# Optimization experiments

Hardware: AMD Instinct MI355X
Metric: run time of the kernel (lower is better)

Reference implementation:

```python
import jax, jax.numpy as jnp
import numpy as np

B, S, E, H = 2, 2048, 1024, 16
D = E // H  # head_dim = 64
EPS = 1e-6


def _angle_decay():
    # angle: 1/10000**linspace(0,1,D//2), each value repeated twice (interleaved)
    a = 1.0 / (10000.0 ** jnp.linspace(0.0, 1.0, D // 2))
    angle = jnp.repeat(a, 2)  # [D]
    decay = jnp.log(1.0 - 2.0 ** (-5.0 - jnp.arange(H, dtype=jnp.float32)))  # [H]
    return angle, decay


def _rel_pos(slen):
    angle, decay = _angle_decay()
    idx = jnp.arange(slen, dtype=jnp.float32)
    sin = jnp.sin(idx[:, None] * angle[None, :])  # [S, D]
    cos = jnp.cos(idx[:, None] * angle[None, :])  # [S, D]
    diff = idx[:, None] - idx[None, :]            # [S, S]
    tril = diff >= 0
    masked = jnp.where(tril, diff, jnp.inf)
    mask = jnp.exp(masked * decay[:, None, None])  # [H, S, S]; exp(-inf)=0 on upper tri
    mask = jnp.nan_to_num(mask)
    mask = mask / jnp.sqrt(jnp.sum(mask, axis=-1, keepdims=True))
    return sin, cos, mask


def _rotate_every_two(x):
    x1 = x[..., ::2]
    x2 = x[..., 1::2]
    return jnp.stack((-x2, x1), axis=-1).reshape(x.shape)


def _theta_shift(x, sin, cos):
    # x: [B, H, S, D]; sin/cos: [S, D] broadcast over B,H
    return x * cos + _rotate_every_two(x) * sin


def setup_inputs() -> dict:
    key = jax.random.key(0)
    ks = jax.random.split(key, 5)
    scale = 1.0 / np.sqrt(E)
    return {
        "x": jax.random.normal(ks[0], (B, S, E), dtype=jnp.float32),
        "Wq": jax.random.normal(ks[1], (E, E), dtype=jnp.float32) * scale,
        "Wk": jax.random.normal(ks[2], (E, E), dtype=jnp.float32) * scale,
        "Wv": jax.random.normal(ks[3], (E, E), dtype=jnp.float32) * scale,
        "Wg": jax.random.normal(ks[4], (E, E), dtype=jnp.float32) * scale,
    }


def reference(x, Wq, Wk, Wv, Wg):
    bsz, tgt_len, _ = x.shape
    sin, cos, mask = _rel_pos(tgt_len)
    scaling = E ** (-0.5)

    q = x @ Wq
    k = (x @ Wk) * scaling
    v = x @ Wv
    g = x @ Wg

    q = q.reshape(bsz, tgt_len, H, D).transpose(0, 2, 1, 3)  # [B,H,S,D]
    k = k.reshape(bsz, tgt_len, H, D).transpose(0, 2, 1, 3)
    vr = v.reshape(bsz, tgt_len, H, D).transpose(0, 2, 1, 3)

    qr = _theta_shift(q, sin, cos)
    kr = _theta_shift(k, sin, cos)

    qk = jnp.einsum("bhqd,bhkd->bhqk", qr, kr) * mask[None]
    denom = jax.lax.stop_gradient(
        jnp.clip(jnp.sum(jnp.abs(qk), axis=-1, keepdims=True), 1.0, 5e4)
    )
    out = jnp.einsum("bhqk,bhkd->bhqd", qk / denom, vr)
    out = out.transpose(0, 2, 1, 3)  # [B,S,H,D]

    # RMSNorm over head_dim (no affine)
    out = out * jax.lax.rsqrt(jnp.mean(out * out, axis=-1, keepdims=True) + EPS)
    out = out.reshape(bsz, tgt_len, E)
    return jax.nn.silu(g) * out
```

## Files before the change

kernel.cpp:

```cpp
#include <hip/hip_runtime.h>

typedef unsigned short u16;
typedef unsigned int u32;
typedef __attribute__((ext_vector_type(8))) __bf16 bf16x8;
typedef __attribute__((ext_vector_type(4))) float f32x4;

#define B_SZ   2
#define S_LEN  2048
#define E_DIM  1024
#define NHEAD  16
#define HD     64
#define KDIM   1024
#define NQKV   3072

__device__ __forceinline__ float bf2f(u16 u){
  union { u32 i; float f; } c; c.i = ((u32)u) << 16; return c.f;
}
__device__ __forceinline__ u16 f2bf(float f){
  union { float f; u32 i; } c; c.f = f;
  return (u16)((c.i + 0x7FFFu + ((c.i >> 16) & 1u)) >> 16);
}
__device__ __forceinline__ u16 f2bf_fast(float f){
  union { float f; u32 i; } c; c.f = f;
  return (u16)((c.i + 0x8000u) >> 16);
}
__device__ __forceinline__ void gl2lds16(const void* g, void* l){
  __builtin_amdgcn_global_load_lds((const __attribute__((address_space(1))) void*)g,
                                   (__attribute__((address_space(3))) void*)l, 16, 0, 0);
}

__global__ __launch_bounds__(256) void prep_kernel(const float* __restrict__ x,
                                                   const float* __restrict__ Wq, const float* __restrict__ Wk,
                                                   const float* __restrict__ Wv, const float* __restrict__ Wg,
                                                   u16* __restrict__ xb, u16* __restrict__ WT){
  __shared__ u16 tile[64][66];
  int z = blockIdx.z;
  int t = threadIdx.x;
  if (z < 4){
    const float* Ws[4] = {Wq, Wk, Wv, Wg};
    const float* W = Ws[z];
    int n0 = blockIdx.x * 64, k0 = blockIdx.y * 64;
    int r = t >> 2, cg = (t & 3) * 16;
    const float* src = W + (size_t)(k0 + r) * E_DIM + n0 + cg;
    float f[16];
    #pragma unroll
    for (int c = 0; c < 4; c++) *(float4*)&f[c * 4] = *(const float4*)&src[c * 4];
    #pragma unroll
    for (int i = 0; i < 16; i++) tile[r][cg + i] = f2bf(f[i]);
    __syncthreads();
    u16 ov[16];
    #pragma unroll
    for (int i = 0; i < 16; i++) ov[i] = tile[cg + i][r];
    int n7 = r & 7, cb = cg >> 3;
    u16* dst = WT + (size_t)(z * E_DIM + n0 + r) * KDIM + k0;
    *(uint4*)&dst[(cb ^ n7) * 8]       = *(uint4*)&ov[0];
    *(uint4*)&dst[((cb + 1) ^ n7) * 8] = *(uint4*)&ov[8];
  } else {
    int blk = (z - 4) * 256 + blockIdx.y * 16 + blockIdx.x;
    size_t flat = ((size_t)blk * 256 + t) * 16;
    int m7 = (int)((flat >> 10) & 7);
    int cb = (int)((flat >> 3) & 7);
    size_t tl = flat & ~(size_t)63;
    float f[16];
    #pragma unroll
    for (int c = 0; c < 4; c++) *(float4*)&f[c * 4] = *(const float4*)&x[flat + c * 4];
    u16 o[16];
    #pragma unroll
    for (int i = 0; i < 16; i++) o[i] = f2bf(f[i]);
    *(uint4*)&xb[tl + ((cb ^ m7) * 8)]       = *(uint4*)&o[0];
    *(uint4*)&xb[tl + (((cb + 1) ^ m7) * 8)] = *(uint4*)&o[8];
  }
}

__global__ __launch_bounds__(256) void gemm_kernel(const u16* __restrict__ A, const u16* __restrict__ Bt,
                                                   u16* __restrict__ qkv, u16* __restrict__ gc){
  __shared__ __align__(16) u16 As[128 * 64];
  __shared__ __align__(16) u16 Bs[128 * 64];
  int m0 = blockIdx.y * 128, n0 = blockIdx.x * 128;
  int t = threadIdx.x;
  int wave = t >> 6, lane = t & 63;
  int l15 = lane & 15, quad = lane >> 4, h8 = lane & 7;
  int r0 = (wave & 1) * 64, c0 = (wave >> 1) * 64;
  f32x4 acc[4][4];
  #pragma unroll
  for (int i = 0; i < 4; i++)
    #pragma unroll
    for (int j = 0; j < 4; j++) acc[i][j] = (f32x4){0.f, 0.f, 0.f, 0.f};

  for (int k0 = 0; k0 < KDIM; k0 += 64){
    __syncthreads();
    #pragma unroll
    for (int c = 0; c < 4; c++){
      int L = c * 256 + t;
      gl2lds16(A + (size_t)(m0 + (L >> 3)) * KDIM + k0 + (L & 7) * 8, &As[L * 8]);
    }
    #pragma unroll
    for (int c = 0; c < 4; c++){
      int L = c * 256 + t;
      gl2lds16(Bt + (size_t)(n0 + (L >> 3)) * KDIM + k0 + (L & 7) * 8, &Bs[L * 8]);
    }
    __syncthreads();
    #pragma unroll
    for (int kk = 0; kk < 2; kk++){
      bf16x8 a[4], b[4];
      #pragma unroll
      for (int i = 0; i < 4; i++) a[i] = *(const bf16x8*)&As[(r0 + i * 16 + l15) * 64 + ((kk * 4 + quad) ^ h8) * 8];
      #pragma unroll
      for (int j = 0; j < 4; j++) b[j] = *(const bf16x8*)&Bs[(c0 + j * 16 + l15) * 64 + ((kk * 4 + quad) ^ h8) * 8];
      #pragma unroll
      for (int i = 0; i < 4; i++)
        #pragma unroll
        for (int j = 0; j < 4; j++)
          acc[i][j] = __builtin_amdgcn_mfma_f32_16x16x32_bf16(a[i], b[j], acc[i][j], 0, 0, 0);
    }
  }
  if (n0 < 3072){
    #pragma unroll
    for (int i = 0; i < 4; i++){
      int row = m0 + r0 + i * 16 + quad * 4;
      #pragma unroll
      for (int j = 0; j < 4; j++){
        int col = n0 + c0 + j * 16 + l15;
        #pragma unroll
        for (int r = 0; r < 4; r++)
          qkv[(size_t)(row + r) * NQKV + col] = f2bf(acc[i][j][r]);
      }
    }
  } else {
    #pragma unroll
    for (int i = 0; i < 4; i++){
      int row = m0 + r0 + i * 16 + quad * 4;
      #pragma unroll
      for (int j = 0; j < 4; j++){
        int e = (n0 - 3072) + c0 + j * 16 + l15;
        #pragma unroll
        for (int r = 0; r < 4; r++)
          gc[(size_t)(row + r) * E_DIM + e] = f2bf(acc[i][j][r]);
      }
    }
  }
}

__global__ __launch_bounds__(256) void shift_kernel(const u16* __restrict__ qkv,
                                                    u16* __restrict__ qr, u16* __restrict__ kr,
                                                    u16* __restrict__ vt){
  int sb = blockIdx.x, bh = blockIdx.y;
  int s0 = sb * 64;
  int t = threadIdx.x;
  int sl = t >> 2, dg = (t & 3) * 16;
  int s = s0 + sl;
  int h = bh & 15;
  size_t token = (size_t)(bh >> 4) * S_LEN + s;
  size_t base = token * NQKV + h * HD + dg;
  u16 qv[16], kv[16], vv[16];
  *(uint4*)&qv[0] = *(const uint4*)&qkv[base];
  *(uint4*)&qv[8] = *(const uint4*)&qkv[base + 8];
  *(uint4*)&kv[0] = *(const uint4*)&qkv[base + 1024];
  *(uint4*)&kv[8] = *(const uint4*)&qkv[base + 1024 + 8];
  *(uint4*)&vv[0] = *(const uint4*)&qkv[base + 2048];
  *(uint4*)&vv[8] = *(const uint4*)&qkv[base + 2048 + 8];
  u16 qo[16], ko[16];
  #pragma unroll
  for (int i = 0; i < 8; i++){
    int dd = dg + 2 * i;
    float a = exp2f(-(float)(dd >> 1) * (13.287712379549449f / 31.0f));
    float ang = (float)s * a;
    float sn, cs;
    __sincosf(ang, &sn, &cs);
    float qe = bf2f(qv[2 * i]), qd = bf2f(qv[2 * i + 1]);
    qo[2 * i]     = f2bf(qe * cs - qd * sn);
    qo[2 * i + 1] = f2bf(qd * cs + qe * sn);
    float ke = bf2f(kv[2 * i]) * 0.03125f, kd = bf2f(kv[2 * i + 1]) * 0.03125f;
    ko[2 * i]     = f2bf(ke * cs - kd * sn);
    ko[2 * i + 1] = f2bf(kd * cs + ke * sn);
  }
  size_t dsto = ((size_t)bh * S_LEN + s) * HD;
  *(uint4*)&qr[dsto + dg]     = *(uint4*)&qo[0];
  *(uint4*)&qr[dsto + dg + 8] = *(uint4*)&qo[8];
  int s7 = s & 7, cbk = dg >> 3;
  *(uint4*)&kr[dsto + ((cbk ^ s7) * 8)]       = *(uint4*)&ko[0];
  *(uint4*)&kr[dsto + (((cbk + 1) ^ s7) * 8)] = *(uint4*)&ko[8];
  __shared__ u16 vs[64][66];
  #pragma unroll
  for (int i = 0; i < 16; i++) vs[sl][dg + i] = vv[i];
  __syncthreads();
  int d = t >> 2, jg = (t & 3) * 16;
  u16 ov[16];
  #pragma unroll
  for (int i = 0; i < 16; i++) ov[i] = vs[jg + i][d];
  int d7 = d & 7, cbv = jg >> 3;
  size_t vrow = ((size_t)bh * HD + d) * S_LEN + s0;
  *(uint4*)&vt[vrow + ((cbv ^ d7) * 8)]       = *(uint4*)&ov[0];
  *(uint4*)&vt[vrow + (((cbv + 1) ^ d7) * 8)] = *(uint4*)&ov[8];
}

__global__ __launch_bounds__(256, 2) void retention_kernel(const u16* __restrict__ qr, const u16* __restrict__ kr,
                                                           const u16* __restrict__ vt,
                                                           u16* __restrict__ pO, u16* __restrict__ pBa){
  int bh = blockIdx.x;
  int qb = 15 - (int)blockIdx.y;
  int z  = blockIdx.z;
  int h = bh & 15;
  int q0 = qb * 128;
  __shared__ __align__(16) u16 Ks[2][64 * 64];
  __shared__ __align__(16) u16 Vs[2][64 * 64];
  __shared__ __align__(16) u16 Ps[128 * 72];
  int t = threadIdx.x, wave = t >> 6, lane = t & 63;
  int l15 = lane & 15, quad = lane >> 4, h8 = lane & 7;

  float decay = log1pf(-exp2f(-5.0f - (float)h));
  float negd = -decay;
  float estep = __expf(64.0f * negd);

  int qsE[2], rowb[2];
  #pragma unroll
  for (int e = 0; e < 2; e++){ rowb[e] = wave * 32 + e * 16; qsE[e] = q0 + rowb[e]; }

  bf16x8 qB[2][2];
  #pragma unroll
  for (int e = 0; e < 2; e++){
    size_t qrow = ((size_t)bh * S_LEN + qsE[e] + l15) * HD;
    qB[e][0] = *(const bf16x8*)&qr[qrow + quad * 8];
    qB[e][1] = *(const bf16x8*)&qr[qrow + 32 + quad * 8];
  }

  float win_f = 11.0f / negd;
  int win_i = (win_f > 2.1e9f) ? 0x7f000000 : (int)win_f;
  int nk = 2 * qb + 2;
  int z_lo = (z * nk) >> 2;
  int z_hi = (((z + 1) * nk) >> 2) - 1;
  int kb_lo = z_lo;
  {
    int jmin = q0 - win_i;
    if (jmin > z_lo * 64){ int wlo = jmin >> 6; kb_lo = wlo > z_lo ? wlo : z_lo; }
  }
  int k0s = kb_lo * 64;

  float em1d = expm1f(decay);
  float rfE[2]; int iE[2];
  #pragma unroll
  for (int e = 0; e < 2; e++){
    int i = qsE[e] + l15;
    iE[e] = i;
    float rowsum = expm1f((float)(i + 1) * decay) / em1d;
    rfE[e] = __expf((float)(i - k0s) * decay) * rsqrtf(rowsum);
  }
  float e1 = __expf(negd);
  float c16 = __expf(negd * 16.0f);
  float cbr[4];
  cbr[0] = __expf(negd * (float)(quad * 4));
  cbr[1] = cbr[0] * e1; cbr[2] = cbr[1] * e1; cbr[3] = cbr[2] * e1;

  f32x4 o[2][4];
  #pragma unroll
  for (int e = 0; e < 2; e++)
    #pragma unroll
    for (int dt = 0; dt < 4; dt++) o[e][dt] = (f32x4){0.f, 0.f, 0.f, 0.f};
  float babs[2] = {0.f, 0.f};

  const u16* krbh = kr + (size_t)bh * S_LEN * HD;
  const u16* vtbh = vt + (size_t)bh * HD * S_LEN;

  if (kb_lo <= z_hi){
    {
      int k0 = kb_lo * 64;
      #pragma unroll
      for (int c = 0; c < 2; c++){
        int L = c * 256 + t;
        gl2lds16(krbh + (size_t)k0 * HD + L * 8, &Ks[0][L * 8]);
      }
      #pragma unroll
      for (int c = 0; c < 2; c++){
        int L = c * 256 + t;
        gl2lds16(vtbh + (size_t)(L >> 3) * S_LEN + k0 + (L & 7) * 8, &Vs[0][L * 8]);
      }
    }
    __syncthreads();
    int cur = 0;
    for (int kb = kb_lo; kb <= z_hi; kb++){
      if (kb < z_hi){
        int k0n = (kb + 1) * 64;
        #pragma unroll
        for (int c = 0; c < 2; c++){
          int L = c * 256 + t;
          gl2lds16(krbh + (size_t)k0n * HD + L * 8, &Ks[cur ^ 1][L * 8]);
        }
        #pragma unroll
        for (int c = 0; c < 2; c++){
          int L = c * 256 + t;
          gl2lds16(vtbh + (size_t)(L >> 3) * S_LEN + k0n + (L & 7) * 8, &Vs[cur ^ 1][L * 8]);
        }
      }
      int k0 = kb * 64;
      const u16* KsC = &Ks[cur][0];
      const u16* VsC = &Vs[cur][0];

      bf16x8 kA0[4], kA1[4];
      #pragma unroll
      for (int ct = 0; ct < 4; ct++){
        int rw = (ct * 16 + l15) * 64;
        kA0[ct] = *(const bf16x8*)&KsC[rw + ((quad ^ h8) * 8)];
        kA1[ct] = *(const bf16x8*)&KsC[rw + (((quad + 4) ^ h8) * 8)];
      }
      #pragma unroll
      for (int e = 0; e < 2; e++){
        int qs = qsE[e];
        if (k0 <= qs + 15 && k0 + 63 >= qs - win_i){
          bool diag = (k0 + 64 > qs);
          float cf[4] = {cbr[0], cbr[1], cbr[2], cbr[3]};
          #pragma unroll
          for (int ct = 0; ct < 4; ct++){
            f32x4 zacc = (f32x4){0.f, 0.f, 0.f, 0.f};
            zacc = __builtin_amdgcn_mfma_f32_16x16x32_bf16(kA0[ct], qB[e][0], zacc, 0, 0, 0);
            zacc = __builtin_amdgcn_mfma_f32_16x16x32_bf16(kA1[ct], qB[e][1], zacc, 0, 0, 0);
            u16 pk[4];
            #pragma unroll
            for (int r = 0; r < 4; r++){
              float p = zacc[r] * (rfE[e] * cf[r]);
              if (diag && (k0 + ct * 16 + quad * 4 + r) > iE[e]) p = 0.f;
              babs[e] += fabsf(p);
              pk[r] = f2bf_fast(p);
              cf[r] *= c16;
            }
            u32 lo = (u32)pk[0] | ((u32)pk[1] << 16);
            u32 hi = (u32)pk[2] | ((u32)pk[3] << 16);
            *(uint2*)&Ps[(rowb[e] + l15) * 72 + ct * 16 + quad * 4] = make_uint2(lo, hi);
          }
        }
      }
      #pragma unroll
      for (int e = 0; e < 2; e++){
        int qs = qsE[e];
        if (k0 <= qs + 15 && k0 + 63 >= qs - win_i){
          bf16x8 pB0 = *(const bf16x8*)&Ps[(rowb[e] + l15) * 72 + quad * 8];
          bf16x8 pB1 = *(const bf16x8*)&Ps[(rowb[e] + l15) * 72 + 32 + quad * 8];
          #pragma unroll
          for (int dt = 0; dt < 4; dt++){
            int rw = (dt * 16 + l15) * 64;
            bf16x8 vA0 = *(const bf16x8*)&VsC[rw + ((quad ^ h8) * 8)];
            bf16x8 vA1 = *(const bf16x8*)&VsC[rw + (((quad + 4) ^ h8) * 8)];
            o[e][dt] = __builtin_amdgcn_mfma_f32_16x16x32_bf16(vA0, pB0, o[e][dt], 0, 0, 0);
            o[e][dt] = __builtin_amdgcn_mfma_f32_16x16x32_bf16(vA1, pB1, o[e][dt], 0, 0, 0);
          }
        }
      }
      #pragma unroll
      for (int e = 0; e < 2; e++) rfE[e] *= estep;
      __syncthreads();
      cur ^= 1;
    }
  }

  size_t slot = ((size_t)bh * 16 + qb) * 4 + z;
  u16* po = pO + slot * (4 * 128 * 16);
  #pragma unroll
  for (int e = 0; e < 2; e++){
    float bsum = babs[e];
    bsum += __shfl_xor(bsum, 16);
    bsum += __shfl_xor(bsum, 32);
    if (quad == 0) pBa[slot * 128 + rowb[e] + l15] = f2bf(bsum);
    #pragma unroll
    for (int dt = 0; dt < 4; dt++){
      u16 pk[4];
      #pragma unroll
      for (int r = 0; r < 4; r++) pk[r] = f2bf(o[e][dt][r]);
      *(uint2*)&po[(dt * 128 + rowb[e] + l15) * 16 + quad * 4] = *(uint2*)pk;
    }
  }
}

__global__ __launch_bounds__(128) void combine_kernel(const u16* __restrict__ pO, const u16* __restrict__ pBa,
                                                      const u16* __restrict__ gc, float* __restrict__ out){
  int bh = blockIdx.x, qb = blockIdx.y;
  int b = bh >> 4, h = bh & 15;
  int i = threadIdx.x;
  int s = qb * 128 + i;
  size_t s4 = ((size_t)bh * 16 + qb) * 4;
  float v[64];
  #pragma unroll
  for (int d = 0; d < 64; d++) v[d] = 0.f;
  float bsum = 0.f;
  #pragma unroll
  for (int z = 0; z < 4; z++){
    const u16* pz = pO + (s4 + z) * 8192;
    #pragma unroll
    for (int dt = 0; dt < 4; dt++){
      u16 a[16];
      *(uint4*)&a[0] = *(const uint4*)&pz[(dt * 128 + i) * 16];
      *(uint4*)&a[8] = *(const uint4*)&pz[(dt * 128 + i) * 16 + 8];
      #pragma unroll
      for (int c = 0; c < 16; c++) v[dt * 16 + c] += bf2f(a[c]);
    }
    bsum += bf2f(pBa[(s4 + z) * 128 + i]);
  }
  float dinv = 1.0f / fminf(fmaxf(bsum, 1.0f), 50000.0f);
  float ssq = 0.f;
  #pragma unroll
  for (int d = 0; d < 64; d++){ v[d] *= dinv; ssq += v[d] * v[d]; }
  float rms = rsqrtf(ssq * (1.0f / 64.0f) + 1e-6f);
  size_t gbase = ((size_t)b * S_LEN + s) * E_DIM + h * HD;
  u16 gu[64];
  #pragma unroll
  for (int c = 0; c < 8; c++) *(uint4*)&gu[c * 8] = *(const uint4*)&gc[gbase + c * 8];
  float ov[64];
  #pragma unroll
  for (int d = 0; d < 64; d++){
    float gv = bf2f(gu[d]);
    float sg = gv / (1.0f + __expf(-gv));
    ov[d] = v[d] * rms * sg;
  }
  float* obase = out + ((size_t)b * S_LEN + s) * E_DIM + h * HD;
  #pragma unroll
  for (int c = 0; c < 16; c++) *(float4*)&obase[c * 4] = *(float4*)&ov[c * 4];
}

extern "C" void kernel_launch(void* const* d_in, const int* in_sizes, int n_in,
                              void* d_out, int out_size, void* d_ws, size_t ws_size,
                              hipStream_t stream){
  const float* x  = (const float*)d_in[0];
  const float* Wq = (const float*)d_in[1];
  const float* Wk = (const float*)d_in[2];
  const float* Wv = (const float*)d_in[3];
  const float* Wg = (const float*)d_in[4];
  float* out = (float*)d_out;
  char* ws = (char*)d_ws;
  u16* qkv = (u16*)(ws);
  u16* pO  = (u16*)(ws);
  u16* xb  = (u16*)(ws + (32ull << 20));
  u16* qrp = (u16*)(ws + (32ull << 20));
  u16* WT  = (u16*)(ws + (40ull << 20));
  u16* krp = (u16*)(ws + (40ull << 20));
  u16* vtp = (u16*)(ws + (48ull << 20));
  u16* gcp = (u16*)(ws + (56ull << 20));
  u16* pBa = (u16*)(ws + (64ull << 20));

  prep_kernel     <<<dim3(16, 16, 8),  256, 0, stream>>>(x, Wq, Wk, Wv, Wg, xb, WT);
  gemm_kernel     <<<dim3(32, 32),     256, 0, stream>>>(xb, WT, qkv, gcp);
  shift_kernel    <<<dim3(32, 32),     256, 0, stream>>>(qkv, qrp, krp, vtp);
  retention_kernel<<<dim3(32, 16, 4),  256, 0, stream>>>(qrp, krp, vtp, pO, pBa);
  combine_kernel  <<<dim3(32, 16),     128, 0, stream>>>(pO, pBa, gcp, out);
}
```

Measured before the change: 188.1 us.

## Rewrite projection GEMM as 256x256 double-buffered pipelined kernel with 8 waves

The fused QKV+gate projection GEMM moves from 128x128 tiles with 4 waves and a single LDS buffer to 256x256 tiles with 8 waves and double-buffered LDS. Global-to-LDS loads for the next k-tile are issued in quarters, interleaved with MFMA phases and explicit waitcnt, barrier and priority control. This is meant to hide memory latency and raise data reuse per tile. The grid shrinks to 256 blocks, which may underfill the 256 CUs, and the larger tiles increase register and LDS pressure.

New measurement: 183.8 us. 1.02x faster.

```diff
diff --git a/kernel.cpp b/kernel.cpp
--- a/kernel.cpp
+++ b/kernel.cpp
@@ -72,55 +72,245 @@
   }
 }
 
-__global__ __launch_bounds__(256) void gemm_kernel(const u16* __restrict__ A, const u16* __restrict__ Bt,
-                                                   u16* __restrict__ qkv, u16* __restrict__ gc){
-  __shared__ __align__(16) u16 As[128 * 64];
-  __shared__ __align__(16) u16 Bs[128 * 64];
-  int m0 = blockIdx.y * 128, n0 = blockIdx.x * 128;
+__global__ __launch_bounds__(512, 2) void gemm_kernel(const u16* __restrict__ A, const u16* __restrict__ Bt,
+                                                      u16* __restrict__ qkv, u16* __restrict__ gc){
+  __shared__ __align__(16) u16 As[2][2][128 * 64];
+  __shared__ __align__(16) u16 Bs[2][2][128 * 64];
+  int m0 = blockIdx.y * 256, n0 = blockIdx.x * 256;
   int t = threadIdx.x;
   int wave = t >> 6, lane = t & 63;
   int l15 = lane & 15, quad = lane >> 4, h8 = lane & 7;
-  int r0 = (wave & 1) * 64, c0 = (wave >> 1) * 64;
-  f32x4 acc[4][4];
-  #pragma unroll
-  for (int i = 0; i < 4; i++)
+  int wm = wave >> 2, wn = wave & 3;
+
+  f32x4 acc[8][4];
+  #pragma unroll
+  for (int i = 0; i < 8; i++)
     #pragma unroll
     for (int j = 0; j < 4; j++) acc[i][j] = (f32x4){0.f, 0.f, 0.f, 0.f};
 
-  for (int k0 = 0; k0 < KDIM; k0 += 64){
-    __syncthreads();
-    #pragma unroll
-    for (int c = 0; c < 4; c++){
-      int L = c * 256 + t;
-      gl2lds16(A + (size_t)(m0 + (L >> 3)) * KDIM + k0 + (L & 7) * 8, &As[L * 8]);
-    }
-    #pragma unroll
-    for (int c = 0; c < 4; c++){
-      int L = c * 256 + t;
-      gl2lds16(Bt + (size_t)(n0 + (L >> 3)) * KDIM + k0 + (L & 7) * 8, &Bs[L * 8]);
-    }
-    __syncthreads();
-    #pragma unroll
-    for (int kk = 0; kk < 2; kk++){
-      bf16x8 a[4], b[4];
-      #pragma unroll
-      for (int i = 0; i < 4; i++) a[i] = *(const bf16x8*)&As[(r0 + i * 16 + l15) * 64 + ((kk * 4 + quad) ^ h8) * 8];
-      #pragma unroll
-      for (int j = 0; j < 4; j++) b[j] = *(const bf16x8*)&Bs[(c0 + j * 16 + l15) * 64 + ((kk * 4 + quad) ^ h8) * 8];
-      #pragma unroll
-      for (int i = 0; i < 4; i++)
-        #pragma unroll
-        for (int j = 0; j < 4; j++)
-          acc[i][j] = __builtin_amdgcn_mfma_f32_16x16x32_bf16(a[i], b[j], acc[i][j], 0, 0, 0);
-    }
-  }
+  auto stA = [&](int buf, int half, int kt){
+    const u16* src = A + (size_t)(m0 + half * 128) * KDIM + kt * 64;
+    #pragma unroll
+    for (int c = 0; c < 2; c++){
+      int L = c * 512 + t;
+      gl2lds16(src + (size_t)(L >> 3) * KDIM + (L & 7) * 8, &As[buf][half][L * 8]);
+    }
+  };
+  auto stB = [&](int buf, int half, int kt){
+    const u16* src = Bt + (size_t)(n0 + half * 128) * KDIM + kt * 64;
+    #pragma unroll
+    for (int c = 0; c < 2; c++){
+      int L = c * 512 + t;
+      gl2lds16(src + (size_t)(L >> 3) * KDIM + (L & 7) * 8, &Bs[buf][half][L * 8]);
+    }
+  };
+  auto ldA = [&](int buf, int i, int ks) -> bf16x8 {
+    int r = i * 16 + l15;
+    return *(const bf16x8*)&As[buf][wm][r * 64 + (((ks * 4 + quad) ^ h8) * 8)];
+  };
+  auto ldB = [&](int buf, int j, int ks) -> bf16x8 {
+    int c = (wn & 1) * 64 + j * 16 + l15;
+    return *(const bf16x8*)&Bs[buf][wn >> 1][c * 64 + (((ks * 4 + quad) ^ h8) * 8)];
+  };
+
+  stA(0, 0, 0); stA(0, 1, 0); stB(0, 0, 0); stB(0, 1, 0); stA(1, 0, 1); stA(1, 1, 1);
+  asm volatile("s_waitcnt vmcnt(4)" ::: "memory");
+  __builtin_amdgcn_s_barrier();
+
+  bf16x8 a0[4][2], a1[4][2];
+
+  for (int t2 = 0; t2 < 8; ++t2){
+    int kt0 = 2 * t2;
+    bool more = (t2 < 7);
+
+    {
+      bf16x8 b0[2][2];
+      #pragma unroll
+      for (int i = 0; i < 4; i++){ a0[i][0] = ldA(0, i, 0); a0[i][1] = ldA(0, i, 1); }
+      #pragma unroll
+      for (int j = 0; j < 2; j++){ b0[j][0] = ldB(0, j, 0); b0[j][1] = ldB(0, j, 1); }
+      stB(1, 0, kt0 + 1);
+      __builtin_amdgcn_sched_barrier(0);
+      __builtin_amdgcn_s_barrier();
+      asm volatile("s_waitcnt lgkmcnt(0)" ::: "memory");
+      __builtin_amdgcn_sched_barrier(0);
+      __builtin_amdgcn_s_setprio(1);
+      #pragma unroll
+      for (int i = 0; i < 4; i++)
+        #pragma unroll
+        for (int j = 0; j < 2; j++){
+          acc[i][j] = __builtin_amdgcn_mfma_f32_16x16x32_bf16(a0[i][0], b0[j][0], acc[i][j], 0, 0, 0);
+          acc[i][j] = __builtin_amdgcn_mfma_f32_16x16x32_bf16(a0[i][1], b0[j][1], acc[i][j], 0, 0, 0);
+        }
+      __builtin_amdgcn_s_setprio(0);
+      __builtin_amdgcn_sched_barrier(0);
+      __builtin_amdgcn_s_barrier();
+    }
+    {
+      bf16x8 b1[2][2];
+      #pragma unroll
+      for (int i = 0; i < 4; i++){ a1[i][0] = ldA(0, i + 4, 0); a1[i][1] = ldA(0, i + 4, 1); }
+      #pragma unroll
+      for (int j = 0; j < 2; j++){ b1[j][0] = ldB(0, j + 2, 0); b1[j][1] = ldB(0, j + 2, 1); }
+      stB(1, 1, kt0 + 1);
+      __builtin_amdgcn_sched_barrier(0);
+      __builtin_amdgcn_s_barrier();
+      asm volatile("s_waitcnt lgkmcnt(0)" ::: "memory");
+      __builtin_amdgcn_sched_barrier(0);
+      __builtin_amdgcn_s_setprio(1);
+      #pragma unroll
+      for (int i = 0; i < 4; i++)
+        #pragma unroll
+        for (int j = 0; j < 2; j++){
+          acc[i][j + 2] = __builtin_amdgcn_mfma_f32_16x16x32_bf16(a0[i][0], b1[j][0], acc[i][j + 2], 0, 0, 0);
+          acc[i][j + 2] = __builtin_amdgcn_mfma_f32_16x16x32_bf16(a0[i][1], b1[j][1], acc[i][j + 2], 0, 0, 0);
+        }
+      __builtin_amdgcn_s_setprio(0);
+      __builtin_amdgcn_sched_barrier(0);
+      __builtin_amdgcn_s_barrier();
+    }
+    {
+      bf16x8 b0[2][2];
+      #pragma unroll
+      for (int j = 0; j < 2; j++){ b0[j][0] = ldB(0, j, 0); b0[j][1] = ldB(0, j, 1); }
+      if (more) stA(0, 0, kt0 + 2);
+      __builtin_amdgcn_sched_barrier(0);
+      __builtin_amdgcn_s_barrier();
+      asm volatile("s_waitcnt lgkmcnt(0)" ::: "memory");
+      __builtin_amdgcn_sched_barrier(0);
+      __builtin_amdgcn_s_setprio(1);
+      #pragma unroll
+      for (int i = 0; i < 4; i++)
+        #pragma unroll
+        for (int j = 0; j < 2; j++){
+          acc[i + 4][j] = __builtin_amdgcn_mfma_f32_16x16x32_bf16(a1[i][0], b0[j][0], acc[i + 4][j], 0, 0, 0);
+          acc[i + 4][j] = __builtin_amdgcn_mfma_f32_16x16x32_bf16(a1[i][1], b0[j][1], acc[i + 4][j], 0, 0, 0);
+        }
+      __builtin_amdgcn_s_setprio(0);
+      __builtin_amdgcn_sched_barrier(0);
+      __builtin_amdgcn_s_barrier();
+    }
+    {
+      bf16x8 b1[2][2];
+      #pragma unroll
+      for (int j = 0; j < 2; j++){ b1[j][0] = ldB(0, j + 2, 0); b1[j][1] = ldB(0, j + 2, 1); }
+      if (more) stA(0, 1, kt0 + 2);
+      __builtin_amdgcn_sched_barrier(0);
+      __builtin_amdgcn_s_barrier();
+      asm volatile("s_waitcnt lgkmcnt(0)" ::: "memory");
+      __builtin_amdgcn_sched_barrier(0);
+      __builtin_amdgcn_s_setprio(1);
+      #pragma unroll
+      for (int i = 0; i < 4; i++)
+        #pragma unroll
+        for (int j = 0; j < 2; j++){
+          acc[i + 4][j + 2] = __builtin_amdgcn_mfma_f32_16x16x32_bf16(a1[i][0], b1[j][0], acc[i + 4][j + 2], 0, 0, 0);
+          acc[i + 4][j + 2] = __builtin_amdgcn_mfma_f32_16x16x32_bf16(a1[i][1], b1[j][1], acc[i + 4][j + 2], 0, 0, 0);
+        }
+      __builtin_amdgcn_s_setprio(0);
+      __builtin_amdgcn_sched_barrier(0);
+      if (more) { asm volatile("s_waitcnt vmcnt(4)" ::: "memory"); }
+      else      { asm volatile("s_waitcnt vmcnt(0)" ::: "memory"); }
+      __builtin_amdgcn_s_barrier();
+    }
+    {
+      bf16x8 b0[2][2];
+      #pragma unroll
+      for (int i = 0; i < 4; i++){ a0[i][0] = ldA(1, i, 0); a0[i][1] = ldA(1, i, 1); }
+      #pragma unroll
+      for (int j = 0; j < 2; j++){ b0[j][0] = ldB(1, j, 0); b0[j][1] = ldB(1, j, 1); }
+      if (more) stB(0, 0, kt0 + 2);
+      __builtin_amdgcn_sched_barrier(0);
+      __builtin_amdgcn_s_barrier();
+      asm volatile("s_waitcnt lgkmcnt(0)" ::: "memory");
+      __builtin_amdgcn_sched_barrier(0);
+      __builtin_amdgcn_s_setprio(1);
+      #pragma unroll
+      for (int i = 0; i < 4; i++)
+        #pragma unroll
+        for (int j = 0; j < 2; j++){
+          acc[i][j] = __builtin_amdgcn_mfma_f32_16x16x32_bf16(a0[i][0], b0[j][0], acc[i][j], 0, 0, 0);
+          acc[i][j] = __builtin_amdgcn_mfma_f32_16x16x32_bf16(a0[i][1], b0[j][1], acc[i][j], 0, 0, 0);
+        }
+      __builtin_amdgcn_s_setprio(0);
+      __builtin_amdgcn_sched_barrier(0);
+      __builtin_amdgcn_s_barrier();
+    }
+    {
+      bf16x8 b1[2][2];
+      #pragma unroll
+      for (int i = 0; i < 4; i++){ a1[i][0] = ldA(1, i + 4, 0); a1[i][1] = ldA(1, i + 4, 1); }
+      #pragma unroll
+      for (int j = 0; j < 2; j++){ b1[j][0] = ldB(1, j + 2, 0); b1[j][1] = ldB(1, j + 2, 1); }
+      if (more) stB(0, 1, kt0 + 2);
+      __builtin_amdgcn_sched_barrier(0);
+      __builtin_amdgcn_s_barrier();
+      asm volatile("s_waitcnt lgkmcnt(0)" ::: "memory");
+      __builtin_amdgcn_sched_barrier(0);
+      __builtin_amdgcn_s_setprio(1);
+      #pragma unroll
+      for (int i = 0; i < 4; i++)
+        #pragma unroll
+        for (int j = 0; j < 2; j++){
+          acc[i][j + 2] = __builtin_amdgcn_mfma_f32_16x16x32_bf16(a0[i][0], b1[j][0], acc[i][j + 2], 0, 0, 0);
+          acc[i][j + 2] = __builtin_amdgcn_mfma_f32_16x16x32_bf16(a0[i][1], b1[j][1], acc[i][j + 2], 0, 0, 0);
+        }
+      __builtin_amdgcn_s_setprio(0);
+      __builtin_amdgcn_sched_barrier(0);
+      __builtin_amdgcn_s_barrier();
+    }
+    {
+      bf16x8 b0[2][2];
+      #pragma unroll
+      for (int j = 0; j < 2; j++){ b0[j][0] = ldB(1, j, 0); b0[j][1] = ldB(1, j, 1); }
+      if (more) stA(1, 0, kt0 + 3);
+      __builtin_amdgcn_sched_barrier(0);
+      __builtin_amdgcn_s_barrier();
+      asm volatile("s_waitcnt lgkmcnt(0)" ::: "memory");
+      __builtin_amdgcn_sched_barrier(0);
+      __builtin_amdgcn_s_setprio(1);
+      #pragma unroll
+      for (int i = 0; i < 4; i++)
+        #pragma unroll
+        for (int j = 0; j < 2; j++){
+          acc[i + 4][j] = __builtin_amdgcn_mfma_f32_16x16x32_bf16(a1[i][0], b0[j][0], acc[i + 4][j], 0, 0, 0);
+          acc[i + 4][j] = __builtin_amdgcn_mfma_f32_16x16x32_bf16(a1[i][1], b0[j][1], acc[i + 4][j], 0, 0, 0);
+        }
+      __builtin_amdgcn_s_setprio(0);
+      __builtin_amdgcn_sched_barrier(0);
+      __builtin_amdgcn_s_barrier();
+    }
+    {
+      bf16x8 b1[2][2];
+      #pragma unroll
+      for (int j = 0; j < 2; j++){ b1[j][0] = ldB(1, j + 2, 0); b1[j][1] = ldB(1, j + 2, 1); }
+      if (more) stA(1, 1, kt0 + 3);
+      __builtin_amdgcn_sched_barrier(0);
+      __builtin_amdgcn_s_barrier();
+      asm volatile("s_waitcnt lgkmcnt(0)" ::: "memory");
+      __builtin_amdgcn_sched_barrier(0);
+      __builtin_amdgcn_s_setprio(1);
+      #pragma unroll
+      for (int i = 0; i < 4; i++)
+        #pragma unroll
+        for (int j = 0; j < 2; j++){
+          acc[i + 4][j + 2] = __builtin_amdgcn_mfma_f32_16x16x32_bf16(a1[i][0], b1[j][0], acc[i + 4][j + 2], 0, 0, 0);
+          acc[i + 4][j + 2] = __builtin_amdgcn_mfma_f32_16x16x32_bf16(a1[i][1], b1[j][1], acc[i + 4][j + 2], 0, 0, 0);
+        }
+      __builtin_amdgcn_s_setprio(0);
+      __builtin_amdgcn_sched_barrier(0);
+      if (more) { asm volatile("s_waitcnt vmcnt(4)" ::: "memory"); }
+      __builtin_amdgcn_s_barrier();
+    }
+  }
+
   if (n0 < 3072){
     #pragma unroll
-    for (int i = 0; i < 4; i++){
-      int row = m0 + r0 + i * 16 + quad * 4;
+    for (int i = 0; i < 8; i++){
+      int row = m0 + wm * 128 + i * 16 + quad * 4;
       #pragma unroll
       for (int j = 0; j < 4; j++){
-        int col = n0 + c0 + j * 16 + l15;
+        int col = n0 + wn * 64 + j * 16 + l15;
         #pragma unroll
         for (int r = 0; r < 4; r++)
           qkv[(size_t)(row + r) * NQKV + col] = f2bf(acc[i][j][r]);
@@ -128,11 +318,11 @@
     }
   } else {
     #pragma unroll
-    for (int i = 0; i < 4; i++){
-      int row = m0 + r0 + i * 16 + quad * 4;
+    for (int i = 0; i < 8; i++){
+      int row = m0 + wm * 128 + i * 16 + quad * 4;
       #pragma unroll
       for (int j = 0; j < 4; j++){
-        int e = (n0 - 3072) + c0 + j * 16 + l15;
+        int e = (n0 - 3072) + wn * 64 + j * 16 + l15;
         #pragma unroll
         for (int r = 0; r < 4; r++)
           gc[(size_t)(row + r) * E_DIM + e] = f2bf(acc[i][j][r]);
@@ -435,7 +625,7 @@
   u16* pBa = (u16*)(ws + (64ull << 20));
 
   prep_kernel     <<<dim3(16, 16, 8),  256, 0, stream>>>(x, Wq, Wk, Wv, Wg, xb, WT);
-  gemm_kernel     <<<dim3(32, 32),     256, 0, stream>>>(xb, WT, qkv, gcp);
+  gemm_kernel     <<<dim3(16, 16),     512, 0, stream>>>(xb, WT, qkv, gcp);
   shift_kernel    <<<dim3(32, 32),     256, 0, stream>>>(qkv, qrp, krp, vtp);
   retention_kernel<<<dim3(32, 16, 4),  256, 0, stream>>>(qrp, krp, vtp, pO, pBa);
   combine_kernel  <<<dim3(32, 16),     128, 0, stream>>>(pO, pBa, gcp, out);
```

## Rewrite projection GEMM with 256x256 tiles, 8 waves, double-buffered LDS pipeline

Applied to the files above, without the earlier changes.

The QKV+gate projection GEMM moves from 128x128 tiles with 4 waves to 256x256 tiles with 8 waves. Each wave now computes a 128x64 sub-tile. LDS is double-buffered, so global-to-LDS loads for the next K slice are issued in the middle of MFMA phases, with explicit barriers, sched_barriers and setprio to interleave loads and matrix ops. This is meant to hide global-load latency and raise data reuse per tile. The cost is far fewer blocks (256 vs 1024), heavy register and LDS use (128KB of LDS), and fragile hand-written synchronisation.

Measured after the change: 185.5 us. Within noise of the previous version (-1.4%).

```diff
diff --git a/kernel.cpp b/kernel.cpp
--- a/kernel.cpp
+++ b/kernel.cpp
@@ -72,55 +72,144 @@
   }
 }
 
-__global__ __launch_bounds__(256) void gemm_kernel(const u16* __restrict__ A, const u16* __restrict__ Bt,
-                                                   u16* __restrict__ qkv, u16* __restrict__ gc){
-  __shared__ __align__(16) u16 As[128 * 64];
-  __shared__ __align__(16) u16 Bs[128 * 64];
-  int m0 = blockIdx.y * 128, n0 = blockIdx.x * 128;
+__global__ __launch_bounds__(512, 2) void gemm_kernel(const u16* __restrict__ A, const u16* __restrict__ Bt,
+                                                      u16* __restrict__ qkv, u16* __restrict__ gc){
+  __shared__ __align__(16) u16 As[2][2][128 * 64];
+  __shared__ __align__(16) u16 Bs[2][2][128 * 64];
+  int m0 = blockIdx.y * 256, n0 = blockIdx.x * 256;
   int t = threadIdx.x;
   int wave = t >> 6, lane = t & 63;
   int l15 = lane & 15, quad = lane >> 4, h8 = lane & 7;
-  int r0 = (wave & 1) * 64, c0 = (wave >> 1) * 64;
-  f32x4 acc[4][4];
-  #pragma unroll
-  for (int i = 0; i < 4; i++)
+  int wm = wave >> 2, wn = wave & 3;
+
+  f32x4 acc[8][4];
+  #pragma unroll
+  for (int i = 0; i < 8; i++)
     #pragma unroll
     for (int j = 0; j < 4; j++) acc[i][j] = (f32x4){0.f, 0.f, 0.f, 0.f};
 
-  for (int k0 = 0; k0 < KDIM; k0 += 64){
-    __syncthreads();
-    #pragma unroll
-    for (int c = 0; c < 4; c++){
-      int L = c * 256 + t;
-      gl2lds16(A + (size_t)(m0 + (L >> 3)) * KDIM + k0 + (L & 7) * 8, &As[L * 8]);
-    }
-    #pragma unroll
-    for (int c = 0; c < 4; c++){
-      int L = c * 256 + t;
-      gl2lds16(Bt + (size_t)(n0 + (L >> 3)) * KDIM + k0 + (L & 7) * 8, &Bs[L * 8]);
-    }
-    __syncthreads();
-    #pragma unroll
-    for (int kk = 0; kk < 2; kk++){
-      bf16x8 a[4], b[4];
-      #pragma unroll
-      for (int i = 0; i < 4; i++) a[i] = *(const bf16x8*)&As[(r0 + i * 16 + l15) * 64 + ((kk * 4 + quad) ^ h8) * 8];
-      #pragma unroll
-      for (int j = 0; j < 4; j++) b[j] = *(const bf16x8*)&Bs[(c0 + j * 16 + l15) * 64 + ((kk * 4 + quad) ^ h8) * 8];
-      #pragma unroll
-      for (int i = 0; i < 4; i++)
-        #pragma unroll
-        for (int j = 0; j < 4; j++)
-          acc[i][j] = __builtin_amdgcn_mfma_f32_16x16x32_bf16(a[i], b[j], acc[i][j], 0, 0, 0);
-    }
-  }
+  auto stA = [&](int buf, int half, int kt){
+    const u16* src = A + (size_t)(m0 + half * 128) * KDIM + kt * 64;
+    #pragma unroll
+    for (int c = 0; c < 2; c++){
+      int L = c * 512 + t;
+      gl2lds16(src + (size_t)(L >> 3) * KDIM + (L & 7) * 8, &As[buf][half][L * 8]);
+    }
+  };
+  auto stB = [&](int buf, int half, int kt){
+    const u16* src = Bt + (size_t)(n0 + half * 128) * KDIM + kt * 64;
+    #pragma unroll
+    for (int c = 0; c < 2; c++){
+      int L = c * 512 + t;
+      gl2lds16(src + (size_t)(L >> 3) * KDIM + (L & 7) * 8, &Bs[buf][half][L * 8]);
+    }
+  };
+  auto ldA = [&](int buf, int i, int ks) -> bf16x8 {
+    int r = i * 16 + l15;
+    return *(const bf16x8*)&As[buf][wm][r * 64 + (((ks * 4 + quad) ^ h8) * 8)];
+  };
+  auto ldB = [&](int buf, int j, int ks) -> bf16x8 {
+    int c = (wn & 1) * 64 + j * 16 + l15;
+    return *(const bf16x8*)&Bs[buf][wn >> 1][c * 64 + (((ks * 4 + quad) ^ h8) * 8)];
+  };
+
+  stA(0, 0, 0); stA(0, 1, 0); stB(0, 0, 0); stB(0, 1, 0);
+  asm volatile("s_waitcnt vmcnt(0)" ::: "memory");
+  __builtin_amdgcn_s_barrier();
+
+  bf16x8 a[4][2];
+  bf16x8 bA[2][2];
+  bf16x8 bB[2][2];
+
+  for (int t2 = 0; t2 < 8; ++t2){
+    int kt0 = 2 * t2;
+    bool more = (t2 < 7);
+
+    #pragma unroll
+    for (int half = 0; half < 2; ++half){
+      int buf = half;
+      int oth = buf ^ 1;
+      {
+        #pragma unroll
+        for (int i = 0; i < 4; i++){ a[i][0] = ldA(buf, i, 0); a[i][1] = ldA(buf, i, 1); }
+        #pragma unroll
+        for (int j = 0; j < 2; j++){ bA[j][0] = ldB(buf, j, 0); bA[j][1] = ldB(buf, j, 1); }
+        if (buf == 0){ stA(1, 0, kt0 + 1); stB(1, 0, kt0 + 1); }
+        else if (more){ stA(0, 0, kt0 + 2); stB(0, 0, kt0 + 2); }
+        __builtin_amdgcn_sched_barrier(0);
+        __builtin_amdgcn_s_barrier();
+        asm volatile("s_waitcnt lgkmcnt(0)" ::: "memory");
+        __builtin_amdgcn_sched_barrier(0);
+        __builtin_amdgcn_s_setprio(1);
+        #pragma unroll
+        for (int i = 0; i < 4; i++)
+          #pragma unroll
+          for (int j = 0; j < 2; j++){
+            acc[i][j] = __builtin_amdgcn_mfma_f32_16x16x32_bf16(a[i][0], bA[j][0], acc[i][j], 0, 0, 0);
+            acc[i][j] = __builtin_amdgcn_mfma_f32_16x16x32_bf16(a[i][1], bA[j][1], acc[i][j], 0, 0, 0);
+          }
+        __builtin_amdgcn_s_setprio(0);
+        __builtin_amdgcn_sched_barrier(0);
+        __builtin_amdgcn_s_barrier();
+      }
+      {
+        #pragma unroll
+        for (int j = 0; j < 2; j++){ bB[j][0] = ldB(buf, j + 2, 0); bB[j][1] = ldB(buf, j + 2, 1); }
+        if (buf == 0){ stA(1, 1, kt0 + 1); stB(1, 1, kt0 + 1); }
+        else if (more){ stA(0, 1, kt0 + 2); stB(0, 1, kt0 + 2); }
+        __builtin_amdgcn_sched_barrier(0);
+        __builtin_amdgcn_s_barrier();
+        asm volatile("s_waitcnt lgkmcnt(0)" ::: "memory");
+        __builtin_amdgcn_sched_barrier(0);
+        __builtin_amdgcn_s_setprio(1);
+        #pragma unroll
+        for (int i = 0; i < 4; i++)
+          #pragma unroll
+          for (int j = 0; j < 2; j++){
+            acc[i][j + 2] = __builtin_amdgcn_mfma_f32_16x16x32_bf16(a[i][0], bB[j][0], acc[i][j + 2], 0, 0, 0);
+            acc[i][j + 2] = __builtin_amdgcn_mfma_f32_16x16x32_bf16(a[i][1], bB[j][1], acc[i][j + 2], 0, 0, 0);
+          }
+        __builtin_amdgcn_s_setprio(0);
+        __builtin_amdgcn_sched_barrier(0);
+        __builtin_amdgcn_s_barrier();
+      }
+      {
+        #pragma unroll
+        for (int i = 0; i < 4; i++){ a[i][0] = ldA(buf, i + 4, 0); a[i][1] = ldA(buf, i + 4, 1); }
+        __builtin_amdgcn_sched_barrier(0);
+        __builtin_amdgcn_s_barrier();
+        asm volatile("s_waitcnt lgkmcnt(0)" ::: "memory");
+        __builtin_amdgcn_sched_barrier(0);
+        __builtin_amdgcn_s_setprio(1);
+        #pragma unroll
+        for (int i = 0; i < 4; i++)
+          #pragma unroll
+          for (int j = 0; j < 2; j++){
+            acc[i + 4][j + 2] = __builtin_amdgcn_mfma_f32_16x16x32_bf16(a[i][0], bB[j][0], acc[i + 4][j + 2], 0, 0, 0);
+            acc[i + 4][j + 2] = __builtin_amdgcn_mfma_f32_16x16x32_bf16(a[i][1], bB[j][1], acc[i + 4][j + 2], 0, 0, 0);
+          }
+        #pragma unroll
+        for (int i = 0; i < 4; i++)
+          #pragma unroll
+          for (int j = 0; j < 2; j++){
+            acc[i + 4][j] = __builtin_amdgcn_mfma_f32_16x16x32_bf16(a[i][0], bA[j][0], acc[i + 4][j], 0, 0, 0);
+            acc[i + 4][j] = __builtin_amdgcn_mfma_f32_16x16x32_bf16(a[i][1], bA[j][1], acc[i + 4][j], 0, 0, 0);
+          }
+        __builtin_amdgcn_s_setprio(0);
+        __builtin_amdgcn_sched_barrier(0);
+        if (buf == 0 || more) { asm volatile("s_waitcnt vmcnt(0)" ::: "memory"); }
+        __builtin_amdgcn_s_barrier();
+      }
+    }
+  }
+
   if (n0 < 3072){
     #pragma unroll
-    for (int i = 0; i < 4; i++){
-      int row = m0 + r0 + i * 16 + quad * 4;
+    for (int i = 0; i < 8; i++){
+      int row = m0 + wm * 128 + i * 16 + quad * 4;
       #pragma unroll
       for (int j = 0; j < 4; j++){
-        int col = n0 + c0 + j * 16 + l15;
+        int col = n0 + wn * 64 + j * 16 + l15;
         #pragma unroll
         for (int r = 0; r < 4; r++)
           qkv[(size_t)(row + r) * NQKV + col] = f2bf(acc[i][j][r]);
@@ -128,11 +217,11 @@
     }
   } else {
     #pragma unroll
-    for (int i = 0; i < 4; i++){
-      int row = m0 + r0 + i * 16 + quad * 4;
+    for (int i = 0; i < 8; i++){
+      int row = m0 + wm * 128 + i * 16 + quad * 4;
       #pragma unroll
       for (int j = 0; j < 4; j++){
-        int e = (n0 - 3072) + c0 + j * 16 + l15;
+        int e = (n0 - 3072) + wn * 64 + j * 16 + l15;
         #pragma unroll
         for (int r = 0; r < 4; r++)
           gc[(size_t)(row + r) * E_DIM + e] = f2bf(acc[i][j][r]);
@@ -435,7 +524,7 @@
   u16* pBa = (u16*)(ws + (64ull << 20));
 
   prep_kernel     <<<dim3(16, 16, 8),  256, 0, stream>>>(x, Wq, Wk, Wv, Wg, xb, WT);
-  gemm_kernel     <<<dim3(32, 32),     256, 0, stream>>>(xb, WT, qkv, gcp);
+  gemm_kernel     <<<dim3(16, 16),     512, 0, stream>>>(xb, WT, qkv, gcp);
   shift_kernel    <<<dim3(32, 32),     256, 0, stream>>>(qkv, qrp, krp, vtp);
   retention_kernel<<<dim3(32, 16, 4),  256, 0, stream>>>(qrp, krp, vtp, pO, pBa);
   combine_kernel  <<<dim3(32, 16),     128, 0, stream>>>(pO, pBa, gcp, out);
```
